# Kernel optimization log

Hardware: AMD Instinct MI355X
Metric: run time of the kernel (lower is better)

## Reference

```python
import jax, jax.numpy as jnp
import numpy as np
import math

DIM = 1024
N_HEADS = 16
HEAD_DIM = DIM // N_HEADS


def setup_inputs() -> dict:
    key = jax.random.key(0)
    kx, kk, kq, kv = jax.random.split(key, 4)
    x = jax.random.normal(kx, (4, 2048, DIM), dtype=jnp.float32)
    # torch.rand -> uniform [0,1)
    wk = jax.random.uniform(kk, (N_HEADS, DIM, HEAD_DIM), dtype=jnp.float32)
    wq = jax.random.uniform(kq, (N_HEADS, DIM, HEAD_DIM), dtype=jnp.float32)
    wv = jax.random.uniform(kv, (N_HEADS, DIM, HEAD_DIM), dtype=jnp.float32)
    return {"x": x, "wk": wk, "wq": wq, "wv": wv}


def reference(x, wk, wq, wv):
    # x: [b, l, d]; w*: [n, d, e]
    k = jnp.einsum('bld,nde->bnle', x, wk)
    q = jnp.einsum('bld,nde->bnle', x, wq)
    v = jnp.einsum('bld,nde->bnle', x, wv)
    head_dim = k.shape[-1]
    scores = jnp.einsum('bnle,bnme->bnlm', q, k) / math.sqrt(head_dim)
    s = jax.nn.softmax(scores, axis=-1)
    r = jnp.einsum('bnlm,bnme->blne', s, v)  # [b, l, n, e]
    b, l, n, e = r.shape
    return r.reshape(b, l, n * e)
```

## Files before the change

kernel.cpp:

```cpp
#include <hip/hip_runtime.h>
#include <math.h>

#define DIMX   1024
#define NHEADS 16
#define HD     64
#define BATCH  4
#define SEQ    2048
#define NM     (BATCH * NHEADS * SEQ * HD)

typedef unsigned short ushort_t;
typedef __attribute__((ext_vector_type(8))) short bf16x8;
typedef __attribute__((ext_vector_type(4))) short bf16x4;
typedef __attribute__((ext_vector_type(4))) float f32x4;

#define MFMA16(a, b, c) __builtin_amdgcn_mfma_f32_16x16x32_bf16(a, b, c, 0, 0, 0)

#if __has_builtin(__builtin_amdgcn_mfma_f32_16x16x16bf16_1k)
#define MFMA_PV(a, b, c) __builtin_amdgcn_mfma_f32_16x16x16bf16_1k(a, b, c, 0, 0, 0)
#else
static __device__ __forceinline__ f32x4 mfma_pv_asm(bf16x4 a, bf16x4 b, f32x4 c) {
    asm("v_mfma_f32_16x16x16_bf16 %0, %1, %2, %0" : "+v"(c) : "v"(a), "v"(b));
    return c;
}
#define MFMA_PV(a, b, c) mfma_pv_asm(a, b, c)
#endif

__device__ __forceinline__ ushort_t f2bf(float x) {
    unsigned u = __float_as_uint(x);
    u += 0x7fffu + ((u >> 16) & 1u);
    return (ushort_t)(u >> 16);
}
__device__ __forceinline__ float bf2f(ushort_t h) {
    return __uint_as_float(((unsigned)h) << 16);
}

__device__ __forceinline__ float fast_exp2(float x) {
#if __has_builtin(__builtin_amdgcn_exp2f)
    return __builtin_amdgcn_exp2f(x);
#else
    return exp2f(x);
#endif
}

#define GLOAD_LDS16(g, l) \
    __builtin_amdgcn_global_load_lds((const __attribute__((address_space(1))) unsigned int*)(g), \
                                     (__attribute__((address_space(3))) unsigned int*)(l), 16, 0, 0)

__global__ __launch_bounds__(256) void convert_x(
    const float* __restrict__ x, ushort_t* __restrict__ Xh, ushort_t* __restrict__ Xl)
{
    int i = blockIdx.x * 256 + threadIdx.x;
    #pragma unroll
    for (int t = 0; t < 4; t++) {
        int idx = t * 524288 + i;
        f32x4 v = ((const f32x4*)x)[idx];
        ushort4 hi, lo;
        hi.x = f2bf(v[0]); lo.x = f2bf(v[0] - bf2f(hi.x));
        hi.y = f2bf(v[1]); lo.y = f2bf(v[1] - bf2f(hi.y));
        hi.z = f2bf(v[2]); lo.z = f2bf(v[2] - bf2f(hi.z));
        hi.w = f2bf(v[3]); lo.w = f2bf(v[3] - bf2f(hi.w));
        ((ushort4*)Xh)[idx] = hi;
        ((ushort4*)Xl)[idx] = lo;
    }
}

__global__ __launch_bounds__(256) void convert_w(
    const float* __restrict__ wk, const float* __restrict__ wq, const float* __restrict__ wv,
    ushort_t* __restrict__ Bqh, ushort_t* __restrict__ Bql, ushort_t* __restrict__ Bvh)
{
    __shared__ float Ts[64][65];
    const int bid = blockIdx.x;
    const int mat = bid >> 8;
    const int rem = bid & 255;
    const int n  = rem >> 4;
    const int dt = rem & 15;
    const float* w = (mat == 0) ? wq : (mat == 1) ? wk : wv;
    const int tid = threadIdx.x;

    #pragma unroll
    for (int t = 0; t < 16; t++) {
        int i = tid + t * 256;
        int r = i >> 6, e = i & 63;
        Ts[r][e] = w[((size_t)n * 1024 + dt * 64 + r) * 64 + e];
    }
    __syncthreads();
    #pragma unroll
    for (int t = 0; t < 16; t++) {
        int i = tid + t * 256;
        int e = i >> 6, r = i & 63;
        float v = Ts[r][e];
        ushort_t hi = f2bf(v);
        size_t o = (size_t)(n * 64 + e) * 1024 + dt * 64 + r;
        if (mat < 2) {
            Bqh[(size_t)mat * 1048576 + o] = hi;
            Bql[(size_t)mat * 1048576 + o] = f2bf(v - bf2f(hi));
        } else {
            Bvh[o] = hi;
        }
    }
}

__global__ __launch_bounds__(256) void proj_qk(
    const ushort_t* __restrict__ Xh, const ushort_t* __restrict__ Xl,
    const ushort_t* __restrict__ Bh, const ushort_t* __restrict__ Bl,
    float* __restrict__ Qf, ushort_t* __restrict__ Khi, ushort_t* __restrict__ Klo)
{
    __shared__ __align__(16) ushort_t Ah[128 * 64];
    __shared__ __align__(16) ushort_t Al[128 * 64];
    __shared__ __align__(16) ushort_t Bhs[128 * 64];
    __shared__ __align__(16) ushort_t Bls[128 * 64];

    const int mt = blockIdx.x, nt = blockIdx.y;
    const int tid = threadIdx.x;
    const int w = tid >> 6, lane = tid & 63, col = lane & 15, quad = lane >> 4;
    const int wm = w & 1, wn = w >> 1;

    f32x4 acc[4][4] = {};

    for (int kc = 0; kc < 1024; kc += 64) {
        __syncthreads();
        #pragma unroll
        for (int i = 0; i < 4; i++) {
            int s = (w * 4 + i) * 64 + lane;
            int r = s >> 3, j = s & 7, g = j ^ (r & 7);
            size_t aoff = (size_t)(mt * 128 + r) * 1024 + kc + g * 8;
            size_t boff = (size_t)(nt * 128 + r) * 1024 + kc + g * 8;
            GLOAD_LDS16(Xh + aoff, Ah  + (size_t)(w * 4 + i) * 512);
            GLOAD_LDS16(Xl + aoff, Al  + (size_t)(w * 4 + i) * 512);
            GLOAD_LDS16(Bh + boff, Bhs + (size_t)(w * 4 + i) * 512);
            GLOAD_LDS16(Bl + boff, Bls + (size_t)(w * 4 + i) * 512);
        }
        __syncthreads();
        #pragma unroll
        for (int kk = 0; kk < 2; kk++) {
            bf16x8 a_h[4], a_l[4], b_h[4], b_l[4];
            const int gi = kk * 4 + quad;
            #pragma unroll
            for (int t = 0; t < 4; t++) {
                int rA = wm * 64 + t * 16 + col;
                int jA = gi ^ (rA & 7);
                a_h[t] = *(const bf16x8*)&Ah[(rA * 8 + jA) * 8];
                a_l[t] = *(const bf16x8*)&Al[(rA * 8 + jA) * 8];
                int rB = wn * 64 + t * 16 + col;
                int jB = gi ^ (rB & 7);
                b_h[t] = *(const bf16x8*)&Bhs[(rB * 8 + jB) * 8];
                b_l[t] = *(const bf16x8*)&Bls[(rB * 8 + jB) * 8];
            }
            #pragma unroll
            for (int t = 0; t < 4; t++)
                #pragma unroll
                for (int u = 0; u < 4; u++) {
                    acc[t][u] = MFMA16(a_h[t], b_h[u], acc[t][u]);
                    acc[t][u] = MFMA16(a_l[t], b_h[u], acc[t][u]);
                    acc[t][u] = MFMA16(a_h[t], b_l[u], acc[t][u]);
                }
        }
    }

    const bool isQ = (nt < 8);
    #pragma unroll
    for (int t = 0; t < 4; t++) {
        #pragma unroll
        for (int u = 0; u < 4; u++) {
            int np = nt * 128 + wn * 64 + u * 16 + col;
            int head = (np >> 6) & 15, e = np & 63;
            #pragma unroll
            for (int rr = 0; rr < 4; rr++) {
                int mm = mt * 128 + wm * 64 + t * 16 + quad * 4 + rr;
                int bi = mm >> 11, l = mm & 2047;
                size_t base = (((size_t)bi * NHEADS + head) * SEQ + l) * HD + e;
                float v = acc[t][u][rr];
                if (isQ) {
                    Qf[base] = v;
                } else {
                    ushort_t hi = f2bf(v);
                    Khi[base] = hi;
                    Klo[base] = f2bf(v - bf2f(hi));
                }
            }
        }
    }
}

__global__ __launch_bounds__(256) void proj_v(
    const ushort_t* __restrict__ Wvh, const ushort_t* __restrict__ Xh,
    ushort_t* __restrict__ Vt)
{
    __shared__ __align__(16) ushort_t Ah[128 * 64];
    __shared__ __align__(16) ushort_t Bhs[128 * 64];

    const int mt = blockIdx.x, nt = blockIdx.y;
    const int tid = threadIdx.x;
    const int w = tid >> 6, lane = tid & 63, col = lane & 15, quad = lane >> 4;
    const int wm = w & 1, wn = w >> 1;

    f32x4 acc[4][4] = {};

    for (int kc = 0; kc < 1024; kc += 64) {
        __syncthreads();
        #pragma unroll
        for (int i = 0; i < 4; i++) {
            int s = (w * 4 + i) * 64 + lane;
            int r = s >> 3, j = s & 7, g = j ^ (r & 7);
            size_t aoff = (size_t)(mt * 128 + r) * 1024 + kc + g * 8;
            size_t boff = (size_t)(nt * 128 + r) * 1024 + kc + g * 8;
            GLOAD_LDS16(Wvh + aoff, Ah  + (size_t)(w * 4 + i) * 512);
            GLOAD_LDS16(Xh  + boff, Bhs + (size_t)(w * 4 + i) * 512);
        }
        __syncthreads();
        #pragma unroll
        for (int kk = 0; kk < 2; kk++) {
            bf16x8 a_h[4], b_h[4];
            const int gi = kk * 4 + quad;
            #pragma unroll
            for (int t = 0; t < 4; t++) {
                int rA = wm * 64 + t * 16 + col;
                a_h[t] = *(const bf16x8*)&Ah[(rA * 8 + (gi ^ (rA & 7))) * 8];
                int rB = wn * 64 + t * 16 + col;
                b_h[t] = *(const bf16x8*)&Bhs[(rB * 8 + (gi ^ (rB & 7))) * 8];
            }
            #pragma unroll
            for (int t = 0; t < 4; t++)
                #pragma unroll
                for (int u = 0; u < 4; u++)
                    acc[t][u] = MFMA16(a_h[t], b_h[u], acc[t][u]);
        }
    }

    #pragma unroll
    for (int t = 0; t < 4; t++) {
        #pragma unroll
        for (int rr = 0; rr < 4; rr++) {
            int ep = mt * 128 + wm * 64 + t * 16 + quad * 4 + rr;
            int head = ep >> 6, e = ep & 63;
            #pragma unroll
            for (int u = 0; u < 4; u++) {
                int lg = nt * 128 + wn * 64 + u * 16 + col;
                int bi = lg >> 11, l = lg & 2047;
                Vt[(((size_t)bi * NHEADS + head) * HD + e) * SEQ + l] = f2bf(acc[t][u][rr]);
            }
        }
    }
}

__global__ __launch_bounds__(256, 2) void attn_mfma_kernel(
    const float* __restrict__ Qf, const ushort_t* __restrict__ Khi,
    const ushort_t* __restrict__ Klo, const ushort_t* __restrict__ Vt,
    float* __restrict__ out)
{
    __shared__ __align__(16) ushort_t Khs[64 * 64];
    __shared__ __align__(16) ushort_t Kls[64 * 64];
    __shared__ __align__(16) ushort_t Vts[64 * 64];

    const int qt  = blockIdx.x;
    const int bn  = blockIdx.y;
    const int tid = threadIdx.x;
    const int w    = tid >> 6;
    const int lane = tid & 63;
    const int col  = lane & 15;
    const int quad = lane >> 4;

    const ushort_t* Kh_g = Khi + (size_t)bn * SEQ * HD;
    const ushort_t* Kl_g = Klo + (size_t)bn * SEQ * HD;
    const ushort_t* Vt_g = Vt  + (size_t)bn * HD * SEQ;

    union { bf16x8 v; short s[8]; } qh[4][2], ql[4][2];
    #pragma unroll
    for (int m = 0; m < 4; m++) {
        const int qrow = qt * 256 + w * 64 + m * 16 + col;
        const float* qp = Qf + ((size_t)bn * SEQ + qrow) * HD;
        #pragma unroll
        for (int ks = 0; ks < 2; ks++) {
            float qv[8];
            f32x4 a = *(const f32x4*)(qp + ks * 32 + quad * 8);
            f32x4 b = *(const f32x4*)(qp + ks * 32 + quad * 8 + 4);
            qv[0]=a[0]; qv[1]=a[1]; qv[2]=a[2]; qv[3]=a[3];
            qv[4]=b[0]; qv[5]=b[1]; qv[6]=b[2]; qv[7]=b[3];
            #pragma unroll
            for (int j = 0; j < 8; j++) {
                float xsc = qv[j] * (0.125f * 1.44269504088896f);
                ushort_t hi = f2bf(xsc);
                ushort_t lo = f2bf(xsc - bf2f(hi));
                qh[m][ks].s[j] = (short)hi;
                ql[m][ks].s[j] = (short)lo;
            }
        }
    }

    f32x4 O[4][4] = {};
    float m_i[4] = {-1e30f, -1e30f, -1e30f, -1e30f};
    float L[4]   = {0.f, 0.f, 0.f, 0.f};

    for (int ch = 0; ch < 32; ch++) {
        __syncthreads();
        #pragma unroll
        for (int t = 0; t < 2; t++) {
            int G   = (w * 2 + t) * 64 + lane;
            int key = G >> 3;
            int blk = (G & 7) ^ (key & 7);
            size_t koff = (size_t)(ch * 64 + key) * HD + blk * 8;
            size_t voff = (size_t)key * SEQ + ch * 64 + blk * 8;
            GLOAD_LDS16(Kh_g + koff, Khs + (w * 2 + t) * 512);
            GLOAD_LDS16(Kl_g + koff, Kls + (w * 2 + t) * 512);
            GLOAD_LDS16(Vt_g + voff, Vts + (w * 2 + t) * 512);
        }
        __syncthreads();

        f32x4 St[4][4] = {};
        #pragma unroll
        for (int ks = 0; ks < 2; ks++) {
            #pragma unroll
            for (int t = 0; t < 4; t++) {
                int key = t * 16 + col;
                int g = key * 8 + ((ks * 4 + quad) ^ (key & 7));
                bf16x8 kh = *(const bf16x8*)&Khs[g * 8];
                bf16x8 kl = *(const bf16x8*)&Kls[g * 8];
                #pragma unroll
                for (int m = 0; m < 4; m++) {
                    St[m][t] = MFMA16(kh, qh[m][ks].v, St[m][t]);
                    St[m][t] = MFMA16(kh, ql[m][ks].v, St[m][t]);
                    St[m][t] = MFMA16(kl, qh[m][ks].v, St[m][t]);
                }
            }
        }

        bf16x4 vfrag[4][4];
        #pragma unroll
        for (int u = 0; u < 4; u++) {
            int rowbase = (u * 16 + col) * 64;
            #pragma unroll
            for (int t = 0; t < 4; t++) {
                int g = (t * 2 + (quad >> 1)) ^ (col & 7);
                vfrag[u][t] = *(const bf16x4*)&Vts[rowbase + g * 8 + (quad & 1) * 4];
            }
        }

        #pragma unroll
        for (int m = 0; m < 4; m++) {
            float mx = St[m][0][0];
            #pragma unroll
            for (int t = 0; t < 4; t++)
                #pragma unroll
                for (int r = 0; r < 4; r++) mx = fmaxf(mx, St[m][t][r]);
            mx = fmaxf(mx, __shfl_xor(mx, 16));
            mx = fmaxf(mx, __shfl_xor(mx, 32));
            float mnew = fmaxf(m_i[m], mx);
            float al   = fast_exp2(m_i[m] - mnew);
            m_i[m] = mnew;

            float psum = 0.f;
            bf16x4 pf[4];
            #pragma unroll
            for (int t = 0; t < 4; t++) {
                #pragma unroll
                for (int r = 0; r < 4; r++) {
                    float p = fast_exp2(St[m][t][r] - mnew);
                    psum += p;
                    pf[t][r] = (short)f2bf(p);
                }
            }
            L[m] = L[m] * al + psum;
            #pragma unroll
            for (int u = 0; u < 4; u++) {
                O[m][u][0] *= al; O[m][u][1] *= al;
                O[m][u][2] *= al; O[m][u][3] *= al;
            }
            #pragma unroll
            for (int t = 0; t < 4; t++)
                #pragma unroll
                for (int u = 0; u < 4; u++)
                    O[m][u] = MFMA_PV(vfrag[u][t], pf[t], O[m][u]);
        }
    }

    const int b = bn >> 4, n = bn & 15;
    #pragma unroll
    for (int m = 0; m < 4; m++) {
        float Lr = L[m];
        Lr += __shfl_xor(Lr, 16);
        Lr += __shfl_xor(Lr, 32);
        float inv = 1.0f / Lr;
        int l = qt * 256 + w * 64 + m * 16 + col;
        size_t base = ((size_t)(b * SEQ + l)) * (NHEADS * HD) + n * HD;
        #pragma unroll
        for (int u = 0; u < 4; u++) {
            f32x4 o;
            o[0] = O[m][u][0] * inv; o[1] = O[m][u][1] * inv;
            o[2] = O[m][u][2] * inv; o[3] = O[m][u][3] * inv;
            *(f32x4*)&out[base + u * 16 + quad * 4] = o;
        }
    }
}

extern "C" void kernel_launch(void* const* d_in, const int* in_sizes, int n_in,
                              void* d_out, int out_size, void* d_ws, size_t ws_size,
                              hipStream_t stream) {
    const float* x  = (const float*)d_in[0];
    const float* wk = (const float*)d_in[1];
    const float* wq = (const float*)d_in[2];
    const float* wv = (const float*)d_in[3];
    float* out = (float*)d_out;

    ushort_t* Xh  = (ushort_t*)d_ws;
    ushort_t* Xl  = Xh + NM;
    ushort_t* Vt  = Xl;
    ushort_t* Bqh = Xl + NM;
    ushort_t* Bql = Bqh + 2097152;
    ushort_t* Bvh = Bql + 2097152;
    float*    Qf  = (float*)(Bvh + 1048576);
    ushort_t* Khi = (ushort_t*)(Qf + NM);
    ushort_t* Klo = Khi + NM;

    convert_x<<<2048, 256, 0, stream>>>(x, Xh, Xl);
    convert_w<<<768, 256, 0, stream>>>(wk, wq, wv, Bqh, Bql, Bvh);
    proj_qk<<<dim3(64, 16), 256, 0, stream>>>(Xh, Xl, Bqh, Bql, Qf, Khi, Klo);
    proj_v<<<dim3(8, 64), 256, 0, stream>>>(Bvh, Xh, Vt);
    attn_mfma_kernel<<<dim3(8, 64), 256, 0, stream>>>(Qf, Khi, Klo, Vt, out);
}
```

Measured before the change: 383.3 us.

## Double-buffer K/V tiles in LDS and pack softmax probabilities by truncation

The K-hi, K-lo and V tiles in LDS are now double-buffered. The next chunk's global-to-LDS loads are issued right after the barrier, so they overlap with the QK^T and PV MFMA work on the current chunk, and one barrier per iteration is dropped. Softmax probabilities are now converted to bf16 by truncation, packed with a byte-permute instead of per-element round-to-nearest. The row sum accumulates the same truncated values so it stays consistent. In exchange, LDS use per block doubles and P carries slightly more rounding bias.

```diff
diff --git a/kernel.cpp b/kernel.cpp
--- a/kernel.cpp
+++ b/kernel.cpp
@@ -32,6 +32,17 @@
 }
 __device__ __forceinline__ float bf2f(ushort_t h) {
     return __uint_as_float(((unsigned)h) << 16);
+}
+
+__device__ __forceinline__ unsigned pack_bf16_trunc(float lo, float hi) {
+#if __has_builtin(__builtin_amdgcn_perm)
+    return __builtin_amdgcn_perm(__float_as_uint(hi), __float_as_uint(lo), 0x07060302u);
+#else
+    return (__float_as_uint(lo) >> 16) | (__float_as_uint(hi) & 0xFFFF0000u);
+#endif
+}
+__device__ __forceinline__ float trunc_bf(float x) {
+    return __uint_as_float(__float_as_uint(x) & 0xFFFF0000u);
 }
 
 __device__ __forceinline__ float fast_exp2(float x) {
@@ -248,9 +259,9 @@
     const ushort_t* __restrict__ Klo, const ushort_t* __restrict__ Vt,
     float* __restrict__ out)
 {
-    __shared__ __align__(16) ushort_t Khs[64 * 64];
-    __shared__ __align__(16) ushort_t Kls[64 * 64];
-    __shared__ __align__(16) ushort_t Vts[64 * 64];
+    __shared__ __align__(16) ushort_t Khs[2][64 * 64];
+    __shared__ __align__(16) ushort_t Kls[2][64 * 64];
+    __shared__ __align__(16) ushort_t Vts[2][64 * 64];
 
     const int qt  = blockIdx.x;
     const int bn  = blockIdx.y;
@@ -264,6 +275,11 @@
     const ushort_t* Kl_g = Klo + (size_t)bn * SEQ * HD;
     const ushort_t* Vt_g = Vt  + (size_t)bn * HD * SEQ;
 
+    const int G0   = (w * 2 + 0) * 64 + lane;
+    const int G1   = (w * 2 + 1) * 64 + lane;
+    const int key0 = G0 >> 3, blk0 = (G0 & 7) ^ (key0 & 7);
+    const int key1 = G1 >> 3, blk1 = (G1 & 7) ^ (key1 & 7);
+
     union { bf16x8 v; short s[8]; } qh[4][2], ql[4][2];
     #pragma unroll
     for (int m = 0; m < 4; m++) {
@@ -291,20 +307,36 @@
     float m_i[4] = {-1e30f, -1e30f, -1e30f, -1e30f};
     float L[4]   = {0.f, 0.f, 0.f, 0.f};
 
+    {
+        size_t k0 = (size_t)key0 * HD + blk0 * 8;
+        size_t k1 = (size_t)key1 * HD + blk1 * 8;
+        size_t v0 = (size_t)key0 * SEQ + blk0 * 8;
+        size_t v1 = (size_t)key1 * SEQ + blk1 * 8;
+        GLOAD_LDS16(Kh_g + k0, &Khs[0][(w * 2 + 0) * 512]);
+        GLOAD_LDS16(Kh_g + k1, &Khs[0][(w * 2 + 1) * 512]);
+        GLOAD_LDS16(Kl_g + k0, &Kls[0][(w * 2 + 0) * 512]);
+        GLOAD_LDS16(Kl_g + k1, &Kls[0][(w * 2 + 1) * 512]);
+        GLOAD_LDS16(Vt_g + v0, &Vts[0][(w * 2 + 0) * 512]);
+        GLOAD_LDS16(Vt_g + v1, &Vts[0][(w * 2 + 1) * 512]);
+    }
+
     for (int ch = 0; ch < 32; ch++) {
+        const int cur = ch & 1;
         __syncthreads();
-        #pragma unroll
-        for (int t = 0; t < 2; t++) {
-            int G   = (w * 2 + t) * 64 + lane;
-            int key = G >> 3;
-            int blk = (G & 7) ^ (key & 7);
-            size_t koff = (size_t)(ch * 64 + key) * HD + blk * 8;
-            size_t voff = (size_t)key * SEQ + ch * 64 + blk * 8;
-            GLOAD_LDS16(Kh_g + koff, Khs + (w * 2 + t) * 512);
-            GLOAD_LDS16(Kl_g + koff, Kls + (w * 2 + t) * 512);
-            GLOAD_LDS16(Vt_g + voff, Vts + (w * 2 + t) * 512);
-        }
-        __syncthreads();
+
+        if (ch + 1 < 32) {
+            const int nxt = cur ^ 1;
+            size_t k0 = (size_t)((ch + 1) * 64 + key0) * HD + blk0 * 8;
+            size_t k1 = (size_t)((ch + 1) * 64 + key1) * HD + blk1 * 8;
+            size_t v0 = (size_t)key0 * SEQ + (ch + 1) * 64 + blk0 * 8;
+            size_t v1 = (size_t)key1 * SEQ + (ch + 1) * 64 + blk1 * 8;
+            GLOAD_LDS16(Kh_g + k0, &Khs[nxt][(w * 2 + 0) * 512]);
+            GLOAD_LDS16(Kh_g + k1, &Khs[nxt][(w * 2 + 1) * 512]);
+            GLOAD_LDS16(Kl_g + k0, &Kls[nxt][(w * 2 + 0) * 512]);
+            GLOAD_LDS16(Kl_g + k1, &Kls[nxt][(w * 2 + 1) * 512]);
+            GLOAD_LDS16(Vt_g + v0, &Vts[nxt][(w * 2 + 0) * 512]);
+            GLOAD_LDS16(Vt_g + v1, &Vts[nxt][(w * 2 + 1) * 512]);
+        }
 
         f32x4 St[4][4] = {};
         #pragma unroll
@@ -313,8 +345,8 @@
             for (int t = 0; t < 4; t++) {
                 int key = t * 16 + col;
                 int g = key * 8 + ((ks * 4 + quad) ^ (key & 7));
-                bf16x8 kh = *(const bf16x8*)&Khs[g * 8];
-                bf16x8 kl = *(const bf16x8*)&Kls[g * 8];
+                bf16x8 kh = *(const bf16x8*)&Khs[cur][g * 8];
+                bf16x8 kl = *(const bf16x8*)&Kls[cur][g * 8];
                 #pragma unroll
                 for (int m = 0; m < 4; m++) {
                     St[m][t] = MFMA16(kh, qh[m][ks].v, St[m][t]);
@@ -331,7 +363,7 @@
             #pragma unroll
             for (int t = 0; t < 4; t++) {
                 int g = (t * 2 + (quad >> 1)) ^ (col & 7);
-                vfrag[u][t] = *(const bf16x4*)&Vts[rowbase + g * 8 + (quad & 1) * 4];
+                vfrag[u][t] = *(const bf16x4*)&Vts[cur][rowbase + g * 8 + (quad & 1) * 4];
             }
         }
 
@@ -352,12 +384,15 @@
             bf16x4 pf[4];
             #pragma unroll
             for (int t = 0; t < 4; t++) {
-                #pragma unroll
-                for (int r = 0; r < 4; r++) {
-                    float p = fast_exp2(St[m][t][r] - mnew);
-                    psum += p;
-                    pf[t][r] = (short)f2bf(p);
-                }
+                float p0 = fast_exp2(St[m][t][0] - mnew);
+                float p1 = fast_exp2(St[m][t][1] - mnew);
+                float p2 = fast_exp2(St[m][t][2] - mnew);
+                float p3 = fast_exp2(St[m][t][3] - mnew);
+                psum += trunc_bf(p0) + trunc_bf(p1) + trunc_bf(p2) + trunc_bf(p3);
+                union { unsigned u[2]; bf16x4 v; } pk;
+                pk.u[0] = pack_bf16_trunc(p0, p1);
+                pk.u[1] = pack_bf16_trunc(p2, p3);
+                pf[t] = pk.v;
             }
             L[m] = L[m] * al + psum;
             #pragma unroll
```

Measured after the change: 381.5 us. About the same (-0.5%).
